# Kernel tuning notes

Measured on AMD Instinct MI355X. Metric: run time of the kernel, lower is better.

Reference implementation:

```python
import jax, jax.numpy as jnp
import numpy as np

EPS = 1e-12  # matches torch.nn.functional.normalize eps


def setup_inputs() -> dict:
    key = jax.random.key(0)
    inputs = jax.random.normal(key, (128, 64, 64, 32), dtype=jnp.float32)
    return {"inputs": inputs}


def reference(inputs) -> jnp.ndarray:
    B, N = inputs.shape[0], inputs.shape[1]
    x = inputs.reshape(B, N, -1)                       # (B, N, D)
    norm = jnp.linalg.norm(x, axis=2, keepdims=True)   # (B, N, 1)
    att = x / jnp.maximum(norm, EPS)                   # L2-normalized rows
    # full N x N self-similarity per batch element
    sim = jnp.einsum('bnd,bmd->bnm', att, att)         # (B, N, N)
    diag_mean = (att * att).sum(axis=2).sum(axis=1).mean()
    loss = sim.sum(axis=(1, 2)).mean() - diag_mean
    return loss
```

## Files before the change

### kernel.cpp

```cpp
#include <hip/hip_runtime.h>
#include <math.h>

#define BB 128
#define NN 64
#define DD 2048
#define ROWS (BB * NN)

__device__ __forceinline__ float wave_reduce_sum_down(float v) {
    #pragma unroll
    for (int off = 32; off > 0; off >>= 1)
        v += __shfl_down(v, off, 64);
    return v;
}

template<int RPW>
__global__ __launch_bounds__(256) void stream_kernel(
        const float* __restrict__ x,
        float* __restrict__ vseg,
        float* __restrict__ diag_seg,
        unsigned* __restrict__ counter) {
    constexpr int RPB = 4 * RPW;
    constexpr int SEG = NN / RPB;
    const int u = blockIdx.x;
    const int b = u / SEG, s = u % SEG;
    const int t = threadIdx.x;
    const int lane = t & 63, w = t >> 6;

    if (u == 0 && t == 0) *counter = 0;

    const float* xw = x + ((size_t)b * NN + s * RPB + w * RPW) * DD;

    float4 acc[8];
    #pragma unroll
    for (int j = 0; j < 8; ++j) acc[j] = make_float4(0.f, 0.f, 0.f, 0.f);
    float diag = 0.f;

    #pragma unroll
    for (int r = 0; r < RPW; ++r) {
        const float4* p = reinterpret_cast<const float4*>(xw + (size_t)r * DD);
        float4 a[8];
        #pragma unroll
        for (int j = 0; j < 8; ++j) a[j] = p[lane + 64 * j];
        float ss = 0.f;
        #pragma unroll
        for (int j = 0; j < 8; ++j)
            ss += a[j].x * a[j].x + a[j].y * a[j].y
                + a[j].z * a[j].z + a[j].w * a[j].w;
        #pragma unroll
        for (int off = 1; off < 64; off <<= 1)
            ss += __shfl_xor(ss, off, 64);
        const float inv = 1.0f / fmaxf(sqrtf(ss), 1e-12f);
        diag += ss * inv * inv;
        #pragma unroll
        for (int j = 0; j < 8; ++j) {
            acc[j].x = fmaf(a[j].x, inv, acc[j].x);
            acc[j].y = fmaf(a[j].y, inv, acc[j].y);
            acc[j].z = fmaf(a[j].z, inv, acc[j].z);
            acc[j].w = fmaf(a[j].w, inv, acc[j].w);
        }
    }

    __shared__ float lds[4][DD];
    __shared__ float dl[4];
    float4* lw = reinterpret_cast<float4*>(lds[w]);
    #pragma unroll
    for (int j = 0; j < 8; ++j) lw[lane + 64 * j] = acc[j];
    if (lane == 0) dl[w] = diag;
    __syncthreads();

    float4 o0 = make_float4(0.f, 0.f, 0.f, 0.f);
    float4 o1 = make_float4(0.f, 0.f, 0.f, 0.f);
    #pragma unroll
    for (int ww = 0; ww < 4; ++ww) {
        const float4* lr = reinterpret_cast<const float4*>(lds[ww]);
        float4 p0 = lr[t], p1 = lr[t + 256];
        o0.x += p0.x; o0.y += p0.y; o0.z += p0.z; o0.w += p0.w;
        o1.x += p1.x; o1.y += p1.y; o1.z += p1.z; o1.w += p1.w;
    }
    float4* dst = reinterpret_cast<float4*>(vseg + (size_t)u * DD);
    dst[t] = o0;
    dst[t + 256] = o1;
    if (t == 0) diag_seg[u] = dl[0] + dl[1] + dl[2] + dl[3];
}

template<int SEG>
__global__ __launch_bounds__(256) void combine_kernel(
        const float* __restrict__ vseg,
        const float* __restrict__ diag_seg,
        double* __restrict__ partials,
        unsigned* __restrict__ counter,
        float* __restrict__ out) {
    const int b = blockIdx.x;
    const int t = threadIdx.x;
    const int lane = t & 63, wid = t >> 6;

    __shared__ float red[4];
    __shared__ int flag;
    __shared__ double sd[BB];

    float4 c0 = make_float4(0.f, 0.f, 0.f, 0.f);
    float4 c1 = make_float4(0.f, 0.f, 0.f, 0.f);
    #pragma unroll
    for (int o = 0; o < SEG; ++o) {
        const float4* src = reinterpret_cast<const float4*>(
            vseg + (size_t)(b * SEG + o) * DD);
        float4 a0 = src[t], a1 = src[t + 256];
        c0.x += a0.x; c0.y += a0.y; c0.z += a0.z; c0.w += a0.w;
        c1.x += a1.x; c1.y += a1.y; c1.z += a1.z; c1.w += a1.w;
    }
    float p = c0.x * c0.x + c0.y * c0.y + c0.z * c0.z + c0.w * c0.w
            + c1.x * c1.x + c1.y * c1.y + c1.z * c1.z + c1.w * c1.w;
    p = wave_reduce_sum_down(p);
    if (lane == 0) red[wid] = p;
    __syncthreads();

    if (t == 0) {
        double sp = (double)red[0] + (double)red[1]
                  + (double)red[2] + (double)red[3];
        double dp = 0.0;
        #pragma unroll
        for (int o = 0; o < SEG; ++o) dp += (double)diag_seg[b * SEG + o];
        __hip_atomic_store(&partials[b], sp - dp,
                           __ATOMIC_RELAXED, __HIP_MEMORY_SCOPE_AGENT);
        asm volatile("s_waitcnt vmcnt(0)" ::: "memory");
        unsigned old = __hip_atomic_fetch_add(counter, 1u,
                        __ATOMIC_RELAXED, __HIP_MEMORY_SCOPE_AGENT);
        flag = (old == (unsigned)(BB - 1)) ? 1 : 0;
    }
    __syncthreads();
    if (!flag) return;

    if (t < BB)
        sd[t] = __hip_atomic_load(&partials[t],
                        __ATOMIC_RELAXED, __HIP_MEMORY_SCOPE_AGENT);
    __syncthreads();
    #pragma unroll
    for (int off = BB / 2; off > 0; off >>= 1) {
        if (t < off) sd[t] += sd[t + off];
        __syncthreads();
    }
    if (t == 0) out[0] = (float)(sd[0] / (double)BB);
}

extern "C" void kernel_launch(void* const* d_in, const int* in_sizes, int n_in,
                              void* d_out, int out_size, void* d_ws, size_t ws_size,
                              hipStream_t stream) {
    const float* x = (const float*)d_in[0];
    float* out = (float*)d_out;
    char* ws = (char*)d_ws;

    const size_t vbytes = (size_t)512 * DD * 4;
    const size_t need = vbytes + 2048 + 1024 + 4;
    if (ws_size >= need) {
        float* vseg       = (float*)ws;
        float* diag_seg   = (float*)(ws + vbytes);
        double* partials  = (double*)(ws + vbytes + 2048);
        unsigned* counter = (unsigned*)(ws + vbytes + 2048 + 1024);
        stream_kernel<4><<<512, 256, 0, stream>>>(x, vseg, diag_seg, counter);
        combine_kernel<4><<<BB, 256, 0, stream>>>(vseg, diag_seg, partials,
                                                  counter, out);
    } else {
        const size_t vb2 = (size_t)256 * DD * 4;
        float* vseg       = (float*)ws;
        float* diag_seg   = (float*)(ws + vb2);
        double* partials  = (double*)(ws + vb2 + 1024);
        unsigned* counter = (unsigned*)(ws + vb2 + 2048);
        stream_kernel<8><<<256, 256, 0, stream>>>(x, vseg, diag_seg, counter);
        combine_kernel<2><<<BB, 256, 0, stream>>>(vseg, diag_seg, partials,
                                                  counter, out);
    }
}
```

Measured before the change: 21.80 us.

## Fuse stream and combine kernels using per-batch last-block atomic counters

Merges the two launches into one kernel: each block writes its segment sum with relaxed atomic stores, bumps a per-batch counter, and the last block of each batch does the combine and squared-norm reduction. A global counter then picks the final block to average over the batch. This removes the second kernel launch and the inter-kernel gap, but adds a hipMemsetAsync for the counters and atomic 64-bit stores and loads. The fallback path for small workspaces is dropped.

```diff
diff --git a/kernel.cpp b/kernel.cpp
--- a/kernel.cpp
+++ b/kernel.cpp
@@ -4,7 +4,8 @@
 #define BB 128
 #define NN 64
 #define DD 2048
-#define ROWS (BB * NN)
+#define NBLK 512
+#define SEG 4
 
 __device__ __forceinline__ float wave_reduce_sum_down(float v) {
     #pragma unroll
@@ -13,22 +14,29 @@
     return v;
 }
 
-template<int RPW>
-__global__ __launch_bounds__(256) void stream_kernel(
+__device__ __forceinline__ unsigned long long pack2(float a, float b) {
+    return ((unsigned long long)__float_as_uint(b) << 32) |
+            (unsigned long long)__float_as_uint(a);
+}
+__device__ __forceinline__ float2 unpack2(unsigned long long v) {
+    return make_float2(__uint_as_float((unsigned)v),
+                       __uint_as_float((unsigned)(v >> 32)));
+}
+
+__global__ __launch_bounds__(256) void fused_kernel(
         const float* __restrict__ x,
         float* __restrict__ vseg,
         float* __restrict__ diag_seg,
-        unsigned* __restrict__ counter) {
-    constexpr int RPB = 4 * RPW;
-    constexpr int SEG = NN / RPB;
+        double* __restrict__ partials,
+        unsigned* __restrict__ bcnt,
+        unsigned* __restrict__ gcnt,
+        float* __restrict__ out) {
     const int u = blockIdx.x;
-    const int b = u / SEG, s = u % SEG;
+    const int b = u >> 2, s = u & 3;
     const int t = threadIdx.x;
     const int lane = t & 63, w = t >> 6;
 
-    if (u == 0 && t == 0) *counter = 0;
-
-    const float* xw = x + ((size_t)b * NN + s * RPB + w * RPW) * DD;
+    const float* xw = x + ((size_t)b * NN + s * 16 + w * 4) * DD;
 
     float4 acc[8];
     #pragma unroll
@@ -36,7 +44,7 @@
     float diag = 0.f;
 
     #pragma unroll
-    for (int r = 0; r < RPW; ++r) {
+    for (int r = 0; r < 4; ++r) {
         const float4* p = reinterpret_cast<const float4*>(xw + (size_t)r * DD);
         float4 a[8];
         #pragma unroll
@@ -62,6 +70,8 @@
 
     __shared__ float lds[4][DD];
     __shared__ float dl[4];
+    __shared__ float red[4];
+    __shared__ int flag;
     float4* lw = reinterpret_cast<float4*>(lds[w]);
     #pragma unroll
     for (int j = 0; j < 8; ++j) lw[lane + 64 * j] = acc[j];
@@ -73,63 +83,78 @@
     #pragma unroll
     for (int ww = 0; ww < 4; ++ww) {
         const float4* lr = reinterpret_cast<const float4*>(lds[ww]);
-        float4 p0 = lr[t], p1 = lr[t + 256];
-        o0.x += p0.x; o0.y += p0.y; o0.z += p0.z; o0.w += p0.w;
-        o1.x += p1.x; o1.y += p1.y; o1.z += p1.z; o1.w += p1.w;
+        float4 q0 = lr[t], q1 = lr[t + 256];
+        o0.x += q0.x; o0.y += q0.y; o0.z += q0.z; o0.w += q0.w;
+        o1.x += q1.x; o1.y += q1.y; o1.z += q1.z; o1.w += q1.w;
     }
-    float4* dst = reinterpret_cast<float4*>(vseg + (size_t)u * DD);
-    dst[t] = o0;
-    dst[t + 256] = o1;
-    if (t == 0) diag_seg[u] = dl[0] + dl[1] + dl[2] + dl[3];
-}
-
-template<int SEG>
-__global__ __launch_bounds__(256) void combine_kernel(
-        const float* __restrict__ vseg,
-        const float* __restrict__ diag_seg,
-        double* __restrict__ partials,
-        unsigned* __restrict__ counter,
-        float* __restrict__ out) {
-    const int b = blockIdx.x;
-    const int t = threadIdx.x;
-    const int lane = t & 63, wid = t >> 6;
-
-    __shared__ float red[4];
-    __shared__ int flag;
-    __shared__ double sd[BB];
-
-    float4 c0 = make_float4(0.f, 0.f, 0.f, 0.f);
-    float4 c1 = make_float4(0.f, 0.f, 0.f, 0.f);
-    #pragma unroll
-    for (int o = 0; o < SEG; ++o) {
-        const float4* src = reinterpret_cast<const float4*>(
-            vseg + (size_t)(b * SEG + o) * DD);
-        float4 a0 = src[t], a1 = src[t + 256];
-        c0.x += a0.x; c0.y += a0.y; c0.z += a0.z; c0.w += a0.w;
-        c1.x += a1.x; c1.y += a1.y; c1.z += a1.z; c1.w += a1.w;
-    }
-    float p = c0.x * c0.x + c0.y * c0.y + c0.z * c0.z + c0.w * c0.w
-            + c1.x * c1.x + c1.y * c1.y + c1.z * c1.z + c1.w * c1.w;
-    p = wave_reduce_sum_down(p);
-    if (lane == 0) red[wid] = p;
+    unsigned long long* dst =
+        reinterpret_cast<unsigned long long*>(vseg + (size_t)u * DD);
+    __hip_atomic_store(dst + 2 * t,       pack2(o0.x, o0.y),
+                       __ATOMIC_RELAXED, __HIP_MEMORY_SCOPE_AGENT);
+    __hip_atomic_store(dst + 2 * t + 1,   pack2(o0.z, o0.w),
+                       __ATOMIC_RELAXED, __HIP_MEMORY_SCOPE_AGENT);
+    __hip_atomic_store(dst + 2 * t + 512, pack2(o1.x, o1.y),
+                       __ATOMIC_RELAXED, __HIP_MEMORY_SCOPE_AGENT);
+    __hip_atomic_store(dst + 2 * t + 513, pack2(o1.z, o1.w),
+                       __ATOMIC_RELAXED, __HIP_MEMORY_SCOPE_AGENT);
+    if (t == 0)
+        __hip_atomic_store(&diag_seg[u], dl[0] + dl[1] + dl[2] + dl[3],
+                           __ATOMIC_RELAXED, __HIP_MEMORY_SCOPE_AGENT);
+    asm volatile("s_waitcnt vmcnt(0)" ::: "memory");
     __syncthreads();
 
+    if (t == 0) {
+        unsigned old = __hip_atomic_fetch_add(&bcnt[b], 1u,
+                        __ATOMIC_RELAXED, __HIP_MEMORY_SCOPE_AGENT);
+        flag = (old == 3u) ? 1 : 0;
+    }
+    __syncthreads();
+    if (!flag) return;
+
+    {
+        float4 c0 = make_float4(0.f, 0.f, 0.f, 0.f);
+        float4 c1 = make_float4(0.f, 0.f, 0.f, 0.f);
+        #pragma unroll
+        for (int o = 0; o < SEG; ++o) {
+            const unsigned long long* src =
+                reinterpret_cast<const unsigned long long*>(
+                    vseg + (size_t)(b * SEG + o) * DD);
+            float2 l0 = unpack2(__hip_atomic_load(src + 2 * t,
+                            __ATOMIC_RELAXED, __HIP_MEMORY_SCOPE_AGENT));
+            float2 h0 = unpack2(__hip_atomic_load(src + 2 * t + 1,
+                            __ATOMIC_RELAXED, __HIP_MEMORY_SCOPE_AGENT));
+            float2 l1 = unpack2(__hip_atomic_load(src + 2 * t + 512,
+                            __ATOMIC_RELAXED, __HIP_MEMORY_SCOPE_AGENT));
+            float2 h1 = unpack2(__hip_atomic_load(src + 2 * t + 513,
+                            __ATOMIC_RELAXED, __HIP_MEMORY_SCOPE_AGENT));
+            c0.x += l0.x; c0.y += l0.y; c0.z += h0.x; c0.w += h0.y;
+            c1.x += l1.x; c1.y += l1.y; c1.z += h1.x; c1.w += h1.y;
+        }
+        float p = c0.x * c0.x + c0.y * c0.y + c0.z * c0.z + c0.w * c0.w
+                + c1.x * c1.x + c1.y * c1.y + c1.z * c1.z + c1.w * c1.w;
+        p = wave_reduce_sum_down(p);
+        if (lane == 0) red[w] = p;
+    }
+    __syncthreads();
     if (t == 0) {
         double sp = (double)red[0] + (double)red[1]
                   + (double)red[2] + (double)red[3];
         double dp = 0.0;
         #pragma unroll
-        for (int o = 0; o < SEG; ++o) dp += (double)diag_seg[b * SEG + o];
+        for (int o = 0; o < SEG; ++o)
+            dp += (double)__hip_atomic_load(&diag_seg[b * SEG + o],
+                        __ATOMIC_RELAXED, __HIP_MEMORY_SCOPE_AGENT);
         __hip_atomic_store(&partials[b], sp - dp,
                            __ATOMIC_RELAXED, __HIP_MEMORY_SCOPE_AGENT);
         asm volatile("s_waitcnt vmcnt(0)" ::: "memory");
-        unsigned old = __hip_atomic_fetch_add(counter, 1u,
+        unsigned old = __hip_atomic_fetch_add(gcnt, 1u,
                         __ATOMIC_RELAXED, __HIP_MEMORY_SCOPE_AGENT);
         flag = (old == (unsigned)(BB - 1)) ? 1 : 0;
     }
     __syncthreads();
     if (!flag) return;
 
+    __shared__ double sd[BB];
     if (t < BB)
         sd[t] = __hip_atomic_load(&partials[t],
                         __ATOMIC_RELAXED, __HIP_MEMORY_SCOPE_AGENT);
@@ -149,24 +174,14 @@
     float* out = (float*)d_out;
     char* ws = (char*)d_ws;
 
-    const size_t vbytes = (size_t)512 * DD * 4;
-    const size_t need = vbytes + 2048 + 1024 + 4;
-    if (ws_size >= need) {
-        float* vseg       = (float*)ws;
-        float* diag_seg   = (float*)(ws + vbytes);
-        double* partials  = (double*)(ws + vbytes + 2048);
-        unsigned* counter = (unsigned*)(ws + vbytes + 2048 + 1024);
-        stream_kernel<4><<<512, 256, 0, stream>>>(x, vseg, diag_seg, counter);
-        combine_kernel<4><<<BB, 256, 0, stream>>>(vseg, diag_seg, partials,
-                                                  counter, out);
-    } else {
-        const size_t vb2 = (size_t)256 * DD * 4;
-        float* vseg       = (float*)ws;
-        float* diag_seg   = (float*)(ws + vb2);
-        double* partials  = (double*)(ws + vb2 + 1024);
-        unsigned* counter = (unsigned*)(ws + vb2 + 2048);
-        stream_kernel<8><<<256, 256, 0, stream>>>(x, vseg, diag_seg, counter);
-        combine_kernel<2><<<BB, 256, 0, stream>>>(vseg, diag_seg, partials,
-                                                  counter, out);
-    }
+    const size_t vbytes = (size_t)NBLK * DD * 4;
+    float* vseg       = (float*)ws;
+    float* diag_seg   = (float*)(ws + vbytes);
+    double* partials  = (double*)(ws + vbytes + 2048);
+    unsigned* bcnt    = (unsigned*)(ws + vbytes + 2048 + 1024);
+    unsigned* gcnt    = (unsigned*)(ws + vbytes + 2048 + 1024 + 512);
+
+    hipMemsetAsync(bcnt, 0, 516, stream);
+    fused_kernel<<<NBLK, 256, 0, stream>>>(x, vseg, diag_seg, partials,
+                                           bcnt, gcnt, out);
 }
```

Result: slower. 28.82 us (+32.2%).
